# Kernel tuning notes

Hardware: AMD Instinct MI355X
Metric: run time of the kernel (lower is better)

The kernel has to match this reference:

```python
import jax, jax.numpy as jnp
import numpy as np

KERNEL_WIDTH = 0.05      # Gaussian KDE bandwidth (Angstrom)
B_SCAT = 5.803           # neutron scattering length of O (fm)
N_ATOMS = 1024
BOX_L = 25.0
N_BINS = 400


def _trapz(y, x):
    # trapezoidal rule along last axis; x is 1D
    dx = x[1:] - x[:-1]
    return jnp.sum((y[..., 1:] + y[..., :-1]) * 0.5 * dx, axis=-1)


def setup_inputs() -> dict:
    key = jax.random.key(0)
    k1, _ = jax.random.split(key)
    positions = jax.random.uniform(k1, (N_ATOMS, 3), dtype=jnp.float32) * BOX_L
    cell = jnp.eye(3, dtype=jnp.float32) * BOX_L
    r_bins = jnp.linspace(0.1, 10.0, N_BINS, dtype=jnp.float32)
    q_bins = jnp.linspace(0.5, 25.0, N_BINS, dtype=jnp.float32)
    return {"positions": positions, "cell": cell, "r_bins": r_bins, "q_bins": q_bins}


def reference(positions, cell, r_bins, q_bins):
    w = KERNEL_WIDTH
    b = B_SCAT
    N = positions.shape[0]

    # --- minimum-image pairwise distances, upper triangle only (self-pairs) ---
    ii, jj = np.triu_indices(N, k=1)                 # static index sets, P = N(N-1)/2
    diff = positions[jj] - positions[ii]             # (P, 3), matches points_2 - points_1
    cell_inv = jnp.linalg.inv(cell)
    frac = diff @ cell_inv                            # (P, 3) fractional coords
    frac = frac - jnp.round(frac)                     # minimum image convention
    mip = frac @ cell
    d = jnp.sqrt(jnp.sum(mip * mip, axis=-1) + 1e-10)  # (P,) observed distances

    # --- Gaussian KDE binning with window mask (mask == exact exclusion) ---
    min_bin = jnp.min(r_bins) - 3.0 * w
    max_bin = jnp.max(r_bins) + 3.0 * w
    in_win = (d > min_bin) & (d < max_bin)            # (P,)
    norm = 1.0 / (w * jnp.sqrt(2.0 * jnp.pi))
    gauss = jnp.exp(-0.5 * ((r_bins[None, :] - d[:, None]) / w) ** 2) * norm  # (P, n_r)
    summed = jnp.sum(jnp.where(in_win[:, None], gauss, 0.0), axis=0)          # (n_r,)

    vol = jnp.abs(jnp.linalg.det(cell))
    n_pairs = d.shape[0]
    g_partial = vol / n_pairs * summed / (4.0 * jnp.pi * r_bins ** 2)

    # single species: frac=1, coeff = b*b*0.01; G(r) = coeff * (g_partial - 1)
    G = (b * b * 0.01) * (g_partial - 1.0)

    # --- S(Q) = 1 + 4*pi*rho/Q * int r G(r) sin(Qr) dr ---
    rho = N / vol
    integrand = (r_bins[None, :] * G[None, :] *
                 jnp.sin(q_bins[:, None] * r_bins[None, :]) /
                 (q_bins[:, None] + 1e-10))           # (n_q, n_r)
    S = 1.0 + 4.0 * jnp.pi * rho * _trapz(integrand, r_bins)

    # --- F(Q) = Q (S(Q) - 1) ---
    F = q_bins * (S - 1.0)

    return jnp.stack([G, S, F])  # (3, n_bins)
```

## Files before the change

### kernel.cpp

```cpp
#include <hip/hip_runtime.h>
#include <math.h>

#define NBINS_MAX 512
#define NMAX      1024
constexpr float KW       = 0.05f;
constexpr float INV_KW   = 20.0f;
constexpr float GNORM    = 0.3989422804014327f * INV_KW;
constexpr float COEFF    = 0.33674809f;
constexpr float FOUR_PI  = 12.566370614359172f;

constexpr float DELTA     = 5.0e-5f;
constexpr float INV_DELTA = 20000.0f;
#define NFINE (640*1024)
constexpr float GWIN      = 9.0f * KW;

__global__ void __launch_bounds__(256)
pair_scatter_kernel(const float* __restrict__ pos,
                    const float* __restrict__ cell,
                    const float* __restrict__ rbins,
                    int* __restrict__ fine,
                    int N, int nbins)
{
    __shared__ float sh_px[NMAX], sh_py[NMAX], sh_pz[NMAX];
    const int t = threadIdx.x;
    for (int i = t; i < N; i += blockDim.x) {
        sh_px[i] = pos[3*i + 0];
        sh_py[i] = pos[3*i + 1];
        sh_pz[i] = pos[3*i + 2];
    }

    float cm[9];
#pragma unroll
    for (int k = 0; k < 9; ++k) cm[k] = cell[k];
    const float a00 = cm[0], a01 = cm[1], a02 = cm[2];
    const float a10 = cm[3], a11 = cm[4], a12 = cm[5];
    const float a20 = cm[6], a21 = cm[7], a22 = cm[8];
    const float det = a00*(a11*a22 - a12*a21)
                    - a01*(a10*a22 - a12*a20)
                    + a02*(a10*a21 - a11*a20);
    const float id = 1.0f / det;
    float im[9];
    im[0] = (a11*a22 - a12*a21)*id;
    im[1] = (a02*a21 - a01*a22)*id;
    im[2] = (a01*a12 - a02*a11)*id;
    im[3] = (a12*a20 - a10*a22)*id;
    im[4] = (a00*a22 - a02*a20)*id;
    im[5] = (a02*a10 - a00*a12)*id;
    im[6] = (a10*a21 - a11*a20)*id;
    im[7] = (a01*a20 - a00*a21)*id;
    im[8] = (a00*a11 - a01*a10)*id;

    const float r0   = rbins[0];
    const float rend = rbins[nbins - 1];
    const float minb = r0   - 3.0f * KW;
    const float maxb = rend + 3.0f * KW;

    __syncthreads();

    const int A    = blockIdx.x;
    const int B    = N - 1 - A;
    const int cntA = N - 1 - A;
    const int cntB = (B != A) ? A : 0;
    const int tot  = cntA + cntB;

    for (int p = t; p < tot; p += blockDim.x) {
        int i, j;
        if (p < cntA) { i = A; j = A + 1 + p; }
        else          { i = B; j = B + 1 + (p - cntA); }

        const float dx = sh_px[j] - sh_px[i];
        const float dy = sh_py[j] - sh_py[i];
        const float dz = sh_pz[j] - sh_pz[i];
        float fx = dx*im[0] + dy*im[3] + dz*im[6];
        float fy = dx*im[1] + dy*im[4] + dz*im[7];
        float fz = dx*im[2] + dy*im[5] + dz*im[8];
        fx -= rintf(fx); fy -= rintf(fy); fz -= rintf(fz);
        const float mx = fx*cm[0] + fy*cm[3] + fz*cm[6];
        const float my = fx*cm[1] + fy*cm[4] + fz*cm[7];
        const float mz = fx*cm[2] + fy*cm[5] + fz*cm[8];
        const float d  = sqrtf(mx*mx + my*my + mz*mz + 1e-10f);

        if (d > minb && d < maxb) {
            int idx = (int)(d * INV_DELTA);
            if (idx < 0) idx = 0;
            if (idx >= NFINE) idx = NFINE - 1;
            atomicAdd(&fine[idx], 1);
        }
    }
}

__global__ void __launch_bounds__(256)
ghist_kernel(const int* __restrict__ fine,
             const float* __restrict__ cell,
             const float* __restrict__ rbins,
             float* __restrict__ Gws,
             float* __restrict__ out,
             int N, int nbins)
{
    __shared__ float sh_red[4];
    const int k = blockIdx.x;
    const int t = threadIdx.x;

    const float rk  = rbins[k];
    int flo = (int)((rk - GWIN) * INV_DELTA);
    int fhi = (int)((rk + GWIN) * INV_DELTA);
    if (flo < 0) flo = 0;
    if (fhi > NFINE - 1) fhi = NFINE - 1;

    float acc = 0.0f;
    for (int f = flo + t; f <= fhi; f += 256) {
        const int c = fine[f];
        const float df = ((float)f + 0.5f) * DELTA;
        const float u  = (rk - df) * INV_KW;
        acc += (float)c * __expf(-0.5f * u * u);
    }

#pragma unroll
    for (int off = 32; off > 0; off >>= 1)
        acc += __shfl_down(acc, off, 64);
    if ((t & 63) == 0) sh_red[t >> 6] = acc;
    __syncthreads();

    if (t == 0) {
        const float summed = GNORM * (sh_red[0] + sh_red[1] + sh_red[2] + sh_red[3]);
        const float a00 = cell[0], a01 = cell[1], a02 = cell[2];
        const float a10 = cell[3], a11 = cell[4], a12 = cell[5];
        const float a20 = cell[6], a21 = cell[7], a22 = cell[8];
        const float det = a00*(a11*a22 - a12*a21)
                        - a01*(a10*a22 - a12*a20)
                        + a02*(a10*a21 - a11*a20);
        const float vol     = fabsf(det);
        const float n_pairs = 0.5f * (float)N * (float)(N - 1);
        const float pref    = vol / n_pairs;
        const float g = pref * summed / (FOUR_PI * rk * rk);
        const float G = COEFF * (g - 1.0f);
        out[k]  = G;
        Gws[k]  = G;
    }
}

__global__ void __launch_bounds__(256)
sq_kernel(const float* __restrict__ Gws,
          const float* __restrict__ cell,
          const float* __restrict__ rbins,
          const float* __restrict__ qbins,
          float* __restrict__ out,
          int N, int nbins)
{
    __shared__ float sh_G[NBINS_MAX];
    __shared__ float sh_r[NBINS_MAX];
    __shared__ float sh_red[4];
    const int qi = blockIdx.x;
    const int t  = threadIdx.x;

    for (int k = t; k < nbins; k += blockDim.x) {
        sh_G[k] = Gws[k];
        sh_r[k] = rbins[k];
    }
    __syncthreads();

    const float a00 = cell[0], a01 = cell[1], a02 = cell[2];
    const float a10 = cell[3], a11 = cell[4], a12 = cell[5];
    const float a20 = cell[6], a21 = cell[7], a22 = cell[8];
    const float det = a00*(a11*a22 - a12*a21)
                    - a01*(a10*a22 - a12*a20)
                    + a02*(a10*a21 - a11*a20);
    const float vol = fabsf(det);
    const float rho = (float)N / vol;

    const float q    = qbins[qi];
    const float qinv = 1.0f / (q + 1e-10f);
    float acc = 0.0f;
    for (int k = t; k < nbins; k += blockDim.x) {
        const float r    = sh_r[k];
        const float w_lo = (k > 0)         ? (r - sh_r[k - 1]) : 0.0f;
        const float w_hi = (k < nbins - 1) ? (sh_r[k + 1] - r) : 0.0f;
        acc += 0.5f * (w_lo + w_hi) * r * sh_G[k] * __sinf(q * r) * qinv;
    }
#pragma unroll
    for (int off = 32; off > 0; off >>= 1)
        acc += __shfl_down(acc, off, 64);
    if ((t & 63) == 0) sh_red[t >> 6] = acc;
    __syncthreads();
    if (t == 0) {
        const float S = 1.0f + FOUR_PI * rho *
                        (sh_red[0] + sh_red[1] + sh_red[2] + sh_red[3]);
        out[nbins + qi]   = S;
        out[2*nbins + qi] = q * (S - 1.0f);
    }
}

extern "C" void kernel_launch(void* const* d_in, const int* in_sizes, int n_in,
                              void* d_out, int out_size, void* d_ws, size_t ws_size,
                              hipStream_t stream)
{
    const float* pos   = (const float*)d_in[0];
    const float* cell  = (const float*)d_in[1];
    const float* rbins = (const float*)d_in[2];
    const float* qbins = (const float*)d_in[3];
    float* out = (float*)d_out;

    const int N     = in_sizes[0] / 3;
    const int nbins = in_sizes[2];
    const int nrp   = (N + 1) / 2;

    int*   fine = (int*)d_ws;
    float* Gws  = (float*)((char*)d_ws + (size_t)NFINE * sizeof(int));

    hipMemsetAsync(fine, 0, (size_t)NFINE * sizeof(int), stream);
    hipLaunchKernelGGL(pair_scatter_kernel, dim3(nrp), dim3(256), 0, stream,
                       pos, cell, rbins, fine, N, nbins);
    hipLaunchKernelGGL(ghist_kernel, dim3(nbins), dim3(256), 0, stream,
                       fine, cell, rbins, Gws, out, N, nbins);
    hipLaunchKernelGGL(sq_kernel, dim3(nbins), dim3(256), 0, stream,
                       Gws, cell, rbins, qbins, out, N, nbins);
}
```

Before: 90.28 us.

## Fuse memset, pair scatter, histogram and S(Q) into one cooperative kernel

Replaces the memset and three kernel launches with a single cooperative kernel that zeroes the fine histogram, scatters pair distances, smooths into G(r), and integrates S(Q), with grid-wide syncs between phases. It also shrinks the fine histogram from 640K to 256K bins, which is still enough to cover r up to about 10.3. The aim is to remove launch and memset overhead. In exchange it adds three grid.sync barriers, and the S(Q) phase now reads rbins and Gws from global memory instead of shared memory.

```diff
diff --git a/kernel.cpp b/kernel.cpp
--- a/kernel.cpp
+++ b/kernel.cpp
@@ -1,5 +1,8 @@
 #include <hip/hip_runtime.h>
+#include <hip/hip_cooperative_groups.h>
 #include <math.h>
+
+namespace cg = cooperative_groups;
 
 #define NBINS_MAX 512
 #define NMAX      1024
@@ -11,18 +14,32 @@
 
 constexpr float DELTA     = 5.0e-5f;
 constexpr float INV_DELTA = 20000.0f;
-#define NFINE (640*1024)
+#define NFINE (256*1024)
 constexpr float GWIN      = 9.0f * KW;
 
+#define GRID_BLOCKS 512
+
 __global__ void __launch_bounds__(256)
-pair_scatter_kernel(const float* __restrict__ pos,
-                    const float* __restrict__ cell,
-                    const float* __restrict__ rbins,
-                    int* __restrict__ fine,
-                    int N, int nbins)
+fused_spectrum_kernel(const float* __restrict__ pos,
+                      const float* __restrict__ cell,
+                      const float* __restrict__ rbins,
+                      const float* __restrict__ qbins,
+                      int*   __restrict__ fine,
+                      float* __restrict__ Gws,
+                      float* __restrict__ out,
+                      int N, int nbins)
 {
+    cg::grid_group grid = cg::this_grid();
     __shared__ float sh_px[NMAX], sh_py[NMAX], sh_pz[NMAX];
-    const int t = threadIdx.x;
+    __shared__ float sh_red[4];
+
+    const int t    = threadIdx.x;
+    const int b    = blockIdx.x;
+    const int gtid = b * blockDim.x + t;
+    const int gnt  = gridDim.x * blockDim.x;
+
+    for (int f = gtid; f < NFINE; f += gnt) fine[f] = 0;
+
     for (int i = t; i < N; i += blockDim.x) {
         sh_px[i] = pos[3*i + 0];
         sh_py[i] = pos[3*i + 1];
@@ -50,143 +67,108 @@
     im[7] = (a01*a20 - a00*a21)*id;
     im[8] = (a00*a11 - a01*a10)*id;
 
+    const float vol     = fabsf(det);
+    const float n_pairs = 0.5f * (float)N * (float)(N - 1);
+    const float rho     = (float)N / vol;
+    const float pref    = vol / n_pairs;
+
     const float r0   = rbins[0];
     const float rend = rbins[nbins - 1];
     const float minb = r0   - 3.0f * KW;
     const float maxb = rend + 3.0f * KW;
 
-    __syncthreads();
+    __threadfence();
+    grid.sync();
 
-    const int A    = blockIdx.x;
-    const int B    = N - 1 - A;
-    const int cntA = N - 1 - A;
-    const int cntB = (B != A) ? A : 0;
-    const int tot  = cntA + cntB;
+    const int nrp = (N + 1) / 2;
+    for (int rp = b; rp < nrp; rp += gridDim.x) {
+        const int A    = rp;
+        const int B    = N - 1 - rp;
+        const int cntA = N - 1 - A;
+        const int cntB = (B != A) ? A : 0;
+        const int tot  = cntA + cntB;
 
-    for (int p = t; p < tot; p += blockDim.x) {
-        int i, j;
-        if (p < cntA) { i = A; j = A + 1 + p; }
-        else          { i = B; j = B + 1 + (p - cntA); }
+        for (int p = t; p < tot; p += blockDim.x) {
+            int i, j;
+            if (p < cntA) { i = A; j = A + 1 + p; }
+            else          { i = B; j = B + 1 + (p - cntA); }
 
-        const float dx = sh_px[j] - sh_px[i];
-        const float dy = sh_py[j] - sh_py[i];
-        const float dz = sh_pz[j] - sh_pz[i];
-        float fx = dx*im[0] + dy*im[3] + dz*im[6];
-        float fy = dx*im[1] + dy*im[4] + dz*im[7];
-        float fz = dx*im[2] + dy*im[5] + dz*im[8];
-        fx -= rintf(fx); fy -= rintf(fy); fz -= rintf(fz);
-        const float mx = fx*cm[0] + fy*cm[3] + fz*cm[6];
-        const float my = fx*cm[1] + fy*cm[4] + fz*cm[7];
-        const float mz = fx*cm[2] + fy*cm[5] + fz*cm[8];
-        const float d  = sqrtf(mx*mx + my*my + mz*mz + 1e-10f);
+            const float dx = sh_px[j] - sh_px[i];
+            const float dy = sh_py[j] - sh_py[i];
+            const float dz = sh_pz[j] - sh_pz[i];
+            float fx = dx*im[0] + dy*im[3] + dz*im[6];
+            float fy = dx*im[1] + dy*im[4] + dz*im[7];
+            float fz = dx*im[2] + dy*im[5] + dz*im[8];
+            fx -= rintf(fx); fy -= rintf(fy); fz -= rintf(fz);
+            const float mx = fx*cm[0] + fy*cm[3] + fz*cm[6];
+            const float my = fx*cm[1] + fy*cm[4] + fz*cm[7];
+            const float mz = fx*cm[2] + fy*cm[5] + fz*cm[8];
+            const float d  = sqrtf(mx*mx + my*my + mz*mz + 1e-10f);
 
-        if (d > minb && d < maxb) {
-            int idx = (int)(d * INV_DELTA);
-            if (idx < 0) idx = 0;
-            if (idx >= NFINE) idx = NFINE - 1;
-            atomicAdd(&fine[idx], 1);
+            if (d > minb && d < maxb) {
+                int idx = (int)(d * INV_DELTA);
+                if (idx < 0) idx = 0;
+                if (idx >= NFINE) idx = NFINE - 1;
+                atomicAdd(&fine[idx], 1);
+            }
         }
     }
-}
 
-__global__ void __launch_bounds__(256)
-ghist_kernel(const int* __restrict__ fine,
-             const float* __restrict__ cell,
-             const float* __restrict__ rbins,
-             float* __restrict__ Gws,
-             float* __restrict__ out,
-             int N, int nbins)
-{
-    __shared__ float sh_red[4];
-    const int k = blockIdx.x;
-    const int t = threadIdx.x;
+    __threadfence();
+    grid.sync();
 
-    const float rk  = rbins[k];
-    int flo = (int)((rk - GWIN) * INV_DELTA);
-    int fhi = (int)((rk + GWIN) * INV_DELTA);
-    if (flo < 0) flo = 0;
-    if (fhi > NFINE - 1) fhi = NFINE - 1;
+    if (b < nbins) {
+        const float rk = rbins[b];
+        int flo = (int)((rk - GWIN) * INV_DELTA);
+        int fhi = (int)((rk + GWIN) * INV_DELTA);
+        if (flo < 0) flo = 0;
+        if (fhi > NFINE - 1) fhi = NFINE - 1;
 
-    float acc = 0.0f;
-    for (int f = flo + t; f <= fhi; f += 256) {
-        const int c = fine[f];
-        const float df = ((float)f + 0.5f) * DELTA;
-        const float u  = (rk - df) * INV_KW;
-        acc += (float)c * __expf(-0.5f * u * u);
+        float acc = 0.0f;
+        for (int f = flo + t; f <= fhi; f += blockDim.x) {
+            const int   c  = fine[f];
+            const float df = ((float)f + 0.5f) * DELTA;
+            const float u  = (rk - df) * INV_KW;
+            acc += (float)c * __expf(-0.5f * u * u);
+        }
+#pragma unroll
+        for (int off = 32; off > 0; off >>= 1)
+            acc += __shfl_down(acc, off, 64);
+        if ((t & 63) == 0) sh_red[t >> 6] = acc;
+        __syncthreads();
+        if (t == 0) {
+            const float summed = GNORM * (sh_red[0] + sh_red[1] + sh_red[2] + sh_red[3]);
+            const float g = pref * summed / (FOUR_PI * rk * rk);
+            const float G = COEFF * (g - 1.0f);
+            out[b] = G;
+            Gws[b] = G;
+        }
     }
 
+    __threadfence();
+    grid.sync();
+
+    if (b < nbins) {
+        const float q    = qbins[b];
+        const float qinv = 1.0f / (q + 1e-10f);
+        float acc = 0.0f;
+        for (int k = t; k < nbins; k += blockDim.x) {
+            const float r    = rbins[k];
+            const float w_lo = (k > 0)         ? (r - rbins[k - 1]) : 0.0f;
+            const float w_hi = (k < nbins - 1) ? (rbins[k + 1] - r) : 0.0f;
+            acc += 0.5f * (w_lo + w_hi) * r * Gws[k] * __sinf(q * r) * qinv;
+        }
 #pragma unroll
-    for (int off = 32; off > 0; off >>= 1)
-        acc += __shfl_down(acc, off, 64);
-    if ((t & 63) == 0) sh_red[t >> 6] = acc;
-    __syncthreads();
-
-    if (t == 0) {
-        const float summed = GNORM * (sh_red[0] + sh_red[1] + sh_red[2] + sh_red[3]);
-        const float a00 = cell[0], a01 = cell[1], a02 = cell[2];
-        const float a10 = cell[3], a11 = cell[4], a12 = cell[5];
-        const float a20 = cell[6], a21 = cell[7], a22 = cell[8];
-        const float det = a00*(a11*a22 - a12*a21)
-                        - a01*(a10*a22 - a12*a20)
-                        + a02*(a10*a21 - a11*a20);
-        const float vol     = fabsf(det);
-        const float n_pairs = 0.5f * (float)N * (float)(N - 1);
-        const float pref    = vol / n_pairs;
-        const float g = pref * summed / (FOUR_PI * rk * rk);
-        const float G = COEFF * (g - 1.0f);
-        out[k]  = G;
-        Gws[k]  = G;
-    }
-}
-
-__global__ void __launch_bounds__(256)
-sq_kernel(const float* __restrict__ Gws,
-          const float* __restrict__ cell,
-          const float* __restrict__ rbins,
-          const float* __restrict__ qbins,
-          float* __restrict__ out,
-          int N, int nbins)
-{
-    __shared__ float sh_G[NBINS_MAX];
-    __shared__ float sh_r[NBINS_MAX];
-    __shared__ float sh_red[4];
-    const int qi = blockIdx.x;
-    const int t  = threadIdx.x;
-
-    for (int k = t; k < nbins; k += blockDim.x) {
-        sh_G[k] = Gws[k];
-        sh_r[k] = rbins[k];
-    }
-    __syncthreads();
-
-    const float a00 = cell[0], a01 = cell[1], a02 = cell[2];
-    const float a10 = cell[3], a11 = cell[4], a12 = cell[5];
-    const float a20 = cell[6], a21 = cell[7], a22 = cell[8];
-    const float det = a00*(a11*a22 - a12*a21)
-                    - a01*(a10*a22 - a12*a20)
-                    + a02*(a10*a21 - a11*a20);
-    const float vol = fabsf(det);
-    const float rho = (float)N / vol;
-
-    const float q    = qbins[qi];
-    const float qinv = 1.0f / (q + 1e-10f);
-    float acc = 0.0f;
-    for (int k = t; k < nbins; k += blockDim.x) {
-        const float r    = sh_r[k];
-        const float w_lo = (k > 0)         ? (r - sh_r[k - 1]) : 0.0f;
-        const float w_hi = (k < nbins - 1) ? (sh_r[k + 1] - r) : 0.0f;
-        acc += 0.5f * (w_lo + w_hi) * r * sh_G[k] * __sinf(q * r) * qinv;
-    }
-#pragma unroll
-    for (int off = 32; off > 0; off >>= 1)
-        acc += __shfl_down(acc, off, 64);
-    if ((t & 63) == 0) sh_red[t >> 6] = acc;
-    __syncthreads();
-    if (t == 0) {
-        const float S = 1.0f + FOUR_PI * rho *
-                        (sh_red[0] + sh_red[1] + sh_red[2] + sh_red[3]);
-        out[nbins + qi]   = S;
-        out[2*nbins + qi] = q * (S - 1.0f);
+        for (int off = 32; off > 0; off >>= 1)
+            acc += __shfl_down(acc, off, 64);
+        if ((t & 63) == 0) sh_red[t >> 6] = acc;
+        __syncthreads();
+        if (t == 0) {
+            const float S = 1.0f + FOUR_PI * rho *
+                            (sh_red[0] + sh_red[1] + sh_red[2] + sh_red[3]);
+            out[nbins + b]   = S;
+            out[2*nbins + b] = q * (S - 1.0f);
+        }
     }
 }
 
@@ -200,18 +182,17 @@
     const float* qbins = (const float*)d_in[3];
     float* out = (float*)d_out;
 
-    const int N     = in_sizes[0] / 3;
-    const int nbins = in_sizes[2];
-    const int nrp   = (N + 1) / 2;
+    int N     = in_sizes[0] / 3;
+    int nbins = in_sizes[2];
 
     int*   fine = (int*)d_ws;
     float* Gws  = (float*)((char*)d_ws + (size_t)NFINE * sizeof(int));
 
-    hipMemsetAsync(fine, 0, (size_t)NFINE * sizeof(int), stream);
-    hipLaunchKernelGGL(pair_scatter_kernel, dim3(nrp), dim3(256), 0, stream,
-                       pos, cell, rbins, fine, N, nbins);
-    hipLaunchKernelGGL(ghist_kernel, dim3(nbins), dim3(256), 0, stream,
-                       fine, cell, rbins, Gws, out, N, nbins);
-    hipLaunchKernelGGL(sq_kernel, dim3(nbins), dim3(256), 0, stream,
-                       Gws, cell, rbins, qbins, out, N, nbins);
+    void* args[] = { (void*)&pos, (void*)&cell, (void*)&rbins, (void*)&qbins,
+                     (void*)&fine, (void*)&Gws, (void*)&out,
+                     (void*)&N, (void*)&nbins };
+
+    hipLaunchCooperativeKernel((void*)fused_spectrum_kernel,
+                               dim3(GRID_BLOCKS), dim3(256),
+                               args, 0, stream);
 }
```

New measurement: 340.1 us. 277% more time.
